# Optimization experiments

Measured on AMD Instinct MI355X. Metric: run time of the kernel, lower is better.

The kernel has to match this reference:

```python
import jax, jax.numpy as jnp
import numpy as np

N = 50000          # nodes
F = 128            # feature dim (indim = outdim)
AVG_DEG = 12       # random edges per node (plus one self-loop)
AVG_D_LOG = 2.6    # avg_d['log'] used by PNA scalers
EPS = 1e-5         # PNA std epsilon / BatchNorm eps


def setup_inputs() -> dict:
    key = jax.random.key(0)
    k1, k2, k3, k4 = jax.random.split(key, 4)
    h = jax.random.normal(k1, (N, F), dtype=jnp.float32)
    E_rand = N * AVG_DEG
    src_r = jax.random.randint(k2, (E_rand,), 0, N)
    dst_r = jax.random.randint(k3, (E_rand,), 0, N)
    loop = jnp.arange(N)
    src = jnp.concatenate([src_r, loop]).astype(jnp.int64) if jax.config.jax_enable_x64 else jnp.concatenate([src_r, loop]).astype(jnp.int32)
    dst = jnp.concatenate([dst_r, loop]).astype(src.dtype)
    concat_dim = F * (1 + 4 * 3)  # indim * (1 + n_aggr * n_scalers)
    W = jax.random.normal(k4, (concat_dim, F), dtype=jnp.float32) * (1.0 / np.sqrt(concat_dim))
    b = jnp.zeros((F,), dtype=jnp.float32)
    gamma = jnp.ones((F,), dtype=jnp.float32)
    beta = jnp.zeros((F,), dtype=jnp.float32)
    return {"h": h, "src": src, "dst": dst, "W": W, "b": b, "gamma": gamma, "beta": beta}


def _pna_forward(h, W, b, gamma, beta, src, dst):
    n = h.shape[0]
    m = h[src]                                            # [E, F] gathered mailbox
    deg = jax.ops.segment_sum(jnp.ones(src.shape[0], h.dtype), dst, num_segments=n)
    deg = jnp.maximum(deg, 1.0)[:, None]                  # every node has a self-loop
    s = jax.ops.segment_sum(m, dst, num_segments=n)
    mean = s / deg
    mx = jax.ops.segment_max(m, dst, num_segments=n)
    mn = jax.ops.segment_min(m, dst, num_segments=n)
    mean_sq = jax.ops.segment_sum(m * m, dst, num_segments=n) / deg
    std = jnp.sqrt(jax.nn.relu(mean_sq - mean * mean) + EPS)
    agg = jnp.concatenate([mean, mx, mn, std], axis=1)    # [N, 4F]
    logd = jnp.log(deg + 1.0)                             # [N, 1]
    scaled = jnp.concatenate([agg,
                              agg * (logd / AVG_D_LOG),
                              agg * (AVG_D_LOG / logd)], axis=1)  # [N, 12F]
    hc = jnp.concatenate([h, scaled], axis=1)             # [N, 13F]
    out = hc @ W + b                                      # posttrans (single linear)
    out = jax.nn.relu(out)                                # activation (dropout p=0)
    mu = out.mean(axis=0)                                 # BatchNorm1d, training stats
    var = out.var(axis=0)                                 # biased variance (torch)
    out = gamma * (out - mu) * jax.lax.rsqrt(var + EPS) + beta
    return out


def reference(h, src, dst, W, b, gamma, beta):
    return _pna_forward(h, W, b, gamma, beta, src, dst)
```

## Files before the change

kernel.cpp:

```cpp
#include <hip/hip_runtime.h>
#include <math.h>

#define FDIM 128
#define AVG_D_LOGF 2.6f
#define BN_EPS 1e-5f
#define NK 10

using f32x2 = __attribute__((ext_vector_type(2))) float;
using f32x4 = __attribute__((ext_vector_type(4))) float;
using s16x8 = __attribute__((ext_vector_type(8))) short;
using u16x8 = __attribute__((ext_vector_type(8))) unsigned short;

__device__ __forceinline__ unsigned short f2bf(float x) {
  unsigned int u = __float_as_uint(x);
  u += 0x7FFFu + ((u >> 16) & 1u);
  return (unsigned short)(u >> 16);
}
__device__ __forceinline__ float bf2f(unsigned short u) {
  return __uint_as_float(((unsigned int)u) << 16);
}
__device__ __forceinline__ f32x2 bfpair(unsigned int u) {
  union { uint2 u2; f32x2 f; } c;
  c.u2 = make_uint2(u << 16, u & 0xFFFF0000u);
  return c.f;
}

__device__ __forceinline__ void gload16(const void* g, void* l) {
  __builtin_amdgcn_global_load_lds(
      (const __attribute__((address_space(1))) void*)g,
      (__attribute__((address_space(3))) void*)l, 16, 0, 0);
}

__global__ void prep_kernel(const float* __restrict__ h, unsigned short* __restrict__ hb,
                            const float* __restrict__ W, unsigned short* __restrict__ wBT,
                            const int* __restrict__ dst, int* __restrict__ deg,
                            int w0, int w1, int w2, int K) {
  int i = blockIdx.x * 256 + threadIdx.x;
  if (i < w0) {
    const f32x4* sp = (const f32x4*)h + (size_t)i * 2;
    f32x4 v0 = sp[0], v1 = sp[1];
    u16x8 o;
    o[0] = f2bf(v0[0]); o[1] = f2bf(v0[1]); o[2] = f2bf(v0[2]); o[3] = f2bf(v0[3]);
    o[4] = f2bf(v1[0]); o[5] = f2bf(v1[1]); o[6] = f2bf(v1[2]); o[7] = f2bf(v1[3]);
    *((u16x8*)hb + i) = o;
  } else if (i < w0 + w1) {
    int idx = i - w0;
    int k = idx >> 7, j = idx & 127;
    wBT[(size_t)j * K + k] = f2bf(W[idx]);
  } else if (i < w0 + w1 + w2) {
    atomicAdd(&deg[dst[i - w0 - w1]], 1);
  }
}

__global__ void scan1(const int* __restrict__ deg, int* __restrict__ offs,
                      int* __restrict__ bsums, int n) {
  __shared__ int tmp[256];
  int t = threadIdx.x, i = blockIdx.x * 256 + t;
  int v = (i < n) ? deg[i] : 0;
  tmp[t] = v; __syncthreads();
  for (int d = 1; d < 256; d <<= 1) {
    int x = (t >= d) ? tmp[t - d] : 0;
    __syncthreads();
    tmp[t] += x;
    __syncthreads();
  }
  if (i < n) offs[i] = tmp[t] - v;
  if (t == 255) bsums[blockIdx.x] = tmp[255];
}

__global__ void csr_fill(const int* __restrict__ src, const int* __restrict__ dst,
                         const int* __restrict__ offs, const int* __restrict__ bsums,
                         int* __restrict__ cursor, int* __restrict__ csr, int E, int nb) {
  __shared__ int tmp[256];
  __shared__ int ex[256];
  const int t = threadIdx.x;
  {
    int v = (t < nb) ? bsums[t] : 0;
    tmp[t] = v; __syncthreads();
    for (int d = 1; d < 256; d <<= 1) {
      int x = (t >= d) ? tmp[t - d] : 0;
      __syncthreads();
      tmp[t] += x;
      __syncthreads();
    }
    ex[t] = tmp[t] - v;
    __syncthreads();
  }
  int i = blockIdx.x * 256 + t;
  if (i < E) {
    int d = dst[i];
    int pos = offs[d] + ex[d >> 8] + atomicAdd(&cursor[d], 1);
    csr[pos] = src[i];
  }
}

__global__ __launch_bounds__(256) void agg_kernel(
    const unsigned short* __restrict__ hb, const int* __restrict__ csr,
    const int* __restrict__ offs, const int* __restrict__ bsums,
    unsigned short* __restrict__ aggb, float2* __restrict__ s12a,
    int n, int E, int nb) {
  __shared__ int tmp[256];
  __shared__ int ex[256];
  {
    int t = threadIdx.x;
    int v = (t < nb) ? bsums[t] : 0;
    tmp[t] = v; __syncthreads();
    for (int d = 1; d < 256; d <<= 1) {
      int x = (t >= d) ? tmp[t - d] : 0;
      __syncthreads();
      tmp[t] += x;
      __syncthreads();
    }
    ex[t] = tmp[t] - v;
    __syncthreads();
  }
  const int gw = (blockIdx.x * 256 + threadIdx.x) >> 6;
  const int lane = threadIdx.x & 63;
  if (gw >= n) return;
  const int beg = offs[gw] + ex[gw >> 8];
  const int end = (gw + 1 < n) ? offs[gw + 1] + ex[(gw + 1) >> 8] : E;
  const int sub = lane >> 5;
  const int fl  = lane & 31;
  const uint2* hp2 = (const uint2*)hb;

  f32x2 s[2] = {{0.f, 0.f}, {0.f, 0.f}};
  f32x2 q[2] = {{0.f, 0.f}, {0.f, 0.f}};
  f32x2 mx[2] = {{-INFINITY, -INFINITY}, {-INFINITY, -INFINITY}};
  f32x2 mn[2] = {{INFINITY, INFINITY}, {INFINITY, INFINITY}};

  auto acc1 = [&](uint2 A) {
    f32x2 a0 = bfpair(A.x), a1 = bfpair(A.y);
    s[0] += a0; s[1] += a1;
    q[0] += a0 * a0; q[1] += a1 * a1;
    mx[0] = __builtin_elementwise_max(mx[0], a0);
    mx[1] = __builtin_elementwise_max(mx[1], a1);
    mn[0] = __builtin_elementwise_min(mn[0], a0);
    mn[1] = __builtin_elementwise_min(mn[1], a1);
  };

  const int cnt = end - beg;
  const int pairs = cnt >> 1;
  int p = 0;
  for (; p + 4 <= pairs; p += 4) {
    int base = beg + 2 * p + sub;
    int i0 = csr[base], i1 = csr[base + 2], i2 = csr[base + 4], i3 = csr[base + 6];
    uint2 A = hp2[(size_t)i0 * 32 + fl];
    uint2 B = hp2[(size_t)i1 * 32 + fl];
    uint2 C = hp2[(size_t)i2 * 32 + fl];
    uint2 D = hp2[(size_t)i3 * 32 + fl];
    acc1(A); acc1(B); acc1(C); acc1(D);
  }
  for (; p < pairs; ++p) {
    int i0 = csr[beg + 2 * p + sub];
    acc1(hp2[(size_t)i0 * 32 + fl]);
  }
  if ((cnt & 1) && sub == 0) {
    int i0 = csr[end - 1];
    acc1(hp2[(size_t)i0 * 32 + fl]);
  }

  #pragma unroll
  for (int k = 0; k < 2; ++k) {
    s[k][0] += __shfl_xor(s[k][0], 32);  s[k][1] += __shfl_xor(s[k][1], 32);
    q[k][0] += __shfl_xor(q[k][0], 32);  q[k][1] += __shfl_xor(q[k][1], 32);
    mx[k][0] = fmaxf(mx[k][0], __shfl_xor(mx[k][0], 32));
    mx[k][1] = fmaxf(mx[k][1], __shfl_xor(mx[k][1], 32));
    mn[k][0] = fminf(mn[k][0], __shfl_xor(mn[k][0], 32));
    mn[k][1] = fminf(mn[k][1], __shfl_xor(mn[k][1], 32));
  }

  float degf = (float)cnt;
  if (degf < 1.f) degf = 1.f;
  const float inv = 1.f / degf;
  if (sub == 0) {
    f32x2 me0 = s[0] * inv, me1 = s[1] * inv;
    float st0 = sqrtf(fmaxf(q[0][0] * inv - me0[0] * me0[0], 0.f) + BN_EPS);
    float st1 = sqrtf(fmaxf(q[0][1] * inv - me0[1] * me0[1], 0.f) + BN_EPS);
    float st2 = sqrtf(fmaxf(q[1][0] * inv - me1[0] * me1[0], 0.f) + BN_EPS);
    float st3 = sqrtf(fmaxf(q[1][1] * inv - me1[1] * me1[1], 0.f) + BN_EPS);
    unsigned int b = (unsigned int)gw * 512u + (unsigned int)fl * 4u;
    uint2 wme = make_uint2((unsigned int)f2bf(me0[0]) | ((unsigned int)f2bf(me0[1]) << 16),
                           (unsigned int)f2bf(me1[0]) | ((unsigned int)f2bf(me1[1]) << 16));
    uint2 wmx = make_uint2((unsigned int)f2bf(mx[0][0]) | ((unsigned int)f2bf(mx[0][1]) << 16),
                           (unsigned int)f2bf(mx[1][0]) | ((unsigned int)f2bf(mx[1][1]) << 16));
    uint2 wmn = make_uint2((unsigned int)f2bf(mn[0][0]) | ((unsigned int)f2bf(mn[0][1]) << 16),
                           (unsigned int)f2bf(mn[1][0]) | ((unsigned int)f2bf(mn[1][1]) << 16));
    uint2 wst = make_uint2((unsigned int)f2bf(st0) | ((unsigned int)f2bf(st1) << 16),
                           (unsigned int)f2bf(st2) | ((unsigned int)f2bf(st3) << 16));
    *(uint2*)&aggb[b      ] = wme;
    *(uint2*)&aggb[b + 128] = wmx;
    *(uint2*)&aggb[b + 256] = wmn;
    *(uint2*)&aggb[b + 384] = wst;
  }
  if (lane == 0) {
    float logd = logf(degf + 1.f);
    s12a[gw] = make_float2(logd / AVG_D_LOGF, AVG_D_LOGF / logd);
  }
}

__global__ __launch_bounds__(256, 3) void gemm_kernel(
    const unsigned short* __restrict__ hb, const unsigned short* __restrict__ wBT,
    const unsigned short* __restrict__ aggb, const float2* __restrict__ s12a,
    const float* __restrict__ bias, float* __restrict__ out,
    float* __restrict__ bnsum, float* __restrict__ bnsq, int n, int K) {
  __shared__ s16x8 As[1024];
  __shared__ s16x8 Bs[3][512];
  const int t = threadIdx.x;
  const int lane = t & 63;
  const int w = t >> 6;
  const int wr = w >> 1, wc = w & 1;
  const int hi = lane >> 4, lr = lane & 15, rx7 = lr & 7;

  const int nwg = gridDim.x;
  const int q = nwg >> 3, r = nwg & 7;
  const int xcd = blockIdx.x & 7, jj = blockIdx.x >> 3;
  const int bx = (xcd < r ? xcd * (q + 1) : r * (q + 1) + (xcd - r) * q) + jj;

  const int m0 = (bx >> 1) * 128;
  const int n0 = (bx & 1) * 64;

  f32x4 acc[3][4][2] = {};

  auto stage = [&](int ss) {
    const bool ph1 = (ss < 2);
    #pragma unroll
    for (int i = 0; i < 4; ++i) {
      int unit = w * 256 + i * 64 + lane;
      int row = unit >> 3, x = unit & 7;
      int node = m0 + row; if (node >= n) node = n - 1;
      int xo = (x ^ (row & 7)) << 3;
      const unsigned short* src = ph1
          ? hb   + (size_t)node * FDIM + ss * 64 + xo
          : aggb + (size_t)node * 512 + (ss - 2) * 64 + xo;
      gload16(src, &As[w * 256 + i * 64]);
    }
    const int nsec = ph1 ? 1 : 3;
    for (int s = 0; s < nsec; ++s) {
      int koff = ph1 ? ss * 64 : (FDIM + s * 512 + (ss - 2) * 64);
      #pragma unroll
      for (int i = 0; i < 2; ++i) {
        int unit = w * 128 + i * 64 + lane;
        int row = unit >> 3, x = unit & 7;
        const unsigned short* src =
            wBT + (size_t)(n0 + row) * K + koff + ((x ^ (row & 7)) << 3);
        gload16(src, &Bs[s][w * 128 + i * 64]);
      }
    }
  };

  for (int step = 0; step < NK; ++step) {
    stage(step);
    __syncthreads();
    #pragma unroll
    for (int ks = 0; ks < 2; ++ks) {
      s16x8 a[4];
      #pragma unroll
      for (int m = 0; m < 4; ++m) {
        int row = wr * 64 + m * 16 + lr;
        a[m] = As[row * 8 + ((ks * 4 + hi) ^ rx7)];
      }
      #pragma unroll
      for (int s = 0; s < 3; ++s) {
        if (step < 2 && s > 0) continue;
        int rb = wc * 32 + lr;
        s16x8 b0 = Bs[s][rb * 8 + ((ks * 4 + hi) ^ rx7)];
        s16x8 b1 = Bs[s][(rb + 16) * 8 + ((ks * 4 + hi) ^ rx7)];
        #pragma unroll
        for (int m = 0; m < 4; ++m) {
          acc[s][m][0] = __builtin_amdgcn_mfma_f32_16x16x32_bf16(a[m], b0, acc[s][m][0], 0, 0, 0);
          acc[s][m][1] = __builtin_amdgcn_mfma_f32_16x16x32_bf16(a[m], b1, acc[s][m][1], 0, 0, 0);
        }
      }
    }
    __syncthreads();
  }

  float* red = (float*)&As[0];
  if (t < 128) red[t] = 0.f;
  __syncthreads();

  const float bv0 = bias[n0 + wc * 32 + lr];
  const float bv1 = bias[n0 + wc * 32 + 16 + lr];
  float cs[2] = {0.f, 0.f}, cq[2] = {0.f, 0.f};
  #pragma unroll
  for (int m = 0; m < 4; ++m) {
    #pragma unroll
    for (int i = 0; i < 4; ++i) {
      int grow = m0 + wr * 64 + m * 16 + hi * 4 + i;
      if (grow >= n) continue;
      float2 sv = s12a[grow];
      #pragma unroll
      for (int nn = 0; nn < 2; ++nn) {
        float v = acc[0][m][nn][i] + sv.x * acc[1][m][nn][i] + sv.y * acc[2][m][nn][i]
                + (nn ? bv1 : bv0);
        v = fmaxf(v, 0.f);
        out[(size_t)grow * FDIM + n0 + wc * 32 + nn * 16 + lr] = v;
        cs[nn] += v; cq[nn] += v * v;
      }
    }
  }
  #pragma unroll
  for (int nn = 0; nn < 2; ++nn) {
    int lc = wc * 32 + nn * 16 + lr;
    atomicAdd(&red[lc], cs[nn]);
    atomicAdd(&red[64 + lc], cq[nn]);
  }
  __syncthreads();
  if (t < 64)       atomicAdd(&bnsum[n0 + t], red[t]);
  else if (t < 128) atomicAdd(&bnsq[n0 + t - 64], red[t]);
}

__global__ void bn_norm(float* __restrict__ out, const float* __restrict__ bnsum,
                        const float* __restrict__ bnsq, const float* __restrict__ gamma,
                        const float* __restrict__ beta, int n) {
  __shared__ float scs[128], shs[128];
  const int t = threadIdx.x;
  if (t < 128) {
    const float invN = 1.f / (float)n;
    const float mu = bnsum[t] * invN;
    const float var = bnsq[t] * invN - mu * mu;
    const float rs = rsqrtf(var + BN_EPS);
    const float s = gamma[t] * rs;
    scs[t] = s; shs[t] = beta[t] - mu * s;
  }
  __syncthreads();
  const int total = n * 32;
  int idx = blockIdx.x * 256 + t;
  const int c4 = (idx & 31) * 4;
  const float s0 = scs[c4], s1 = scs[c4 + 1], s2 = scs[c4 + 2], s3 = scs[c4 + 3];
  const float h0 = shs[c4], h1 = shs[c4 + 1], h2 = shs[c4 + 2], h3 = shs[c4 + 3];
  for (; idx < total; idx += gridDim.x * 256) {
    f32x4 v = ((f32x4*)out)[idx];
    v[0] = v[0] * s0 + h0;
    v[1] = v[1] * s1 + h1;
    v[2] = v[2] * s2 + h2;
    v[3] = v[3] * s3 + h3;
    ((f32x4*)out)[idx] = v;
  }
}

extern "C" void kernel_launch(void* const* d_in, const int* in_sizes, int n_in,
                              void* d_out, int out_size, void* d_ws, size_t ws_size,
                              hipStream_t stream) {
  const float* h     = (const float*)d_in[0];
  const int*   src   = (const int*)d_in[1];
  const int*   dst   = (const int*)d_in[2];
  const float* W     = (const float*)d_in[3];
  const float* bias  = (const float*)d_in[4];
  const float* gamma = (const float*)d_in[5];
  const float* beta  = (const float*)d_in[6];
  float* out = (float*)d_out;

  const int n = in_sizes[0] / FDIM;
  const int E = in_sizes[1];
  const int K = in_sizes[3] / FDIM;

  char* base = (char*)d_ws;
  size_t off = 0;
  auto alloc = [&](size_t bytes) -> void* {
    void* p = base + off;
    off += (bytes + 255) & ~(size_t)255;
    return p;
  };
  int*   deg    = (int*)  alloc(4ull * n);
  int*   cursor = (int*)  alloc(4ull * n);
  float* bnsum  = (float*)alloc(512);
  float* bnsq   = (float*)alloc(512);
  const size_t zlen = off;
  int*    offs  = (int*)  alloc(4ull * (n + 1));
  int*    bsums = (int*)  alloc(4ull * 256);
  int*    csr   = (int*)  alloc(4ull * E);
  float2* s12a  = (float2*)alloc(8ull * n);
  unsigned short* aggb = (unsigned short*)alloc(2ull * (size_t)n * 512);
  unsigned short* wBT  = (unsigned short*)alloc(2ull * (size_t)K * FDIM);
  unsigned short* hb   = (unsigned short*)alloc(2ull * (size_t)n * FDIM);
  (void)ws_size; (void)n_in; (void)out_size;

  const int eb = (E + 255) / 256;
  const int nb = (n + 255) / 256;
  const int w0 = n * FDIM / 8;
  const int w1 = K * FDIM;
  const int w2 = E;

  hipMemsetAsync(d_ws, 0, zlen, stream);
  prep_kernel<<<(w0 + w1 + w2 + 255) / 256, 256, 0, stream>>>(h, hb, W, wBT, dst, deg,
                                                              w0, w1, w2, K);
  scan1<<<nb, 256, 0, stream>>>(deg, offs, bsums, n);
  csr_fill<<<eb, 256, 0, stream>>>(src, dst, offs, bsums, cursor, csr, E, nb);
  agg_kernel<<<(n + 3) / 4, 256, 0, stream>>>(hb, csr, offs, bsums, aggb, s12a, n, E, nb);
  const int gblocks = ((n + 127) / 128) * 2;
  gemm_kernel<<<gblocks, 256, 0, stream>>>(hb, wBT, aggb, s12a, bias,
                                           out, bnsum, bnsq, n, K);
  bn_norm<<<2048, 256, 0, stream>>>(out, bnsum, bnsq, gamma, beta, n);
}
```

Baseline: 181.4 us.

## Double-buffer GEMM LDS stages and prescale CSR indices for cheaper gathers

The GEMM kernel now double-buffers its A/B shared-memory tiles, issuing the next stage's global-to-LDS loads before computing the current one, with manual vmcnt waits and raw barriers in place of __syncthreads. Occupancy hint drops from 3 to 2 blocks per CU because LDS use doubles. Separately, the CSR stores source indices pre-shifted to byte offsets, so the aggregation gather avoids index multiplication, and the accumulators use inline packed add/fma asm. Risks: hand-counted vmcnt values must match the number of issued loads per stage, and the shifted indices could overflow for very large node counts.

```diff
diff --git a/kernel.cpp b/kernel.cpp
--- a/kernel.cpp
+++ b/kernel.cpp
@@ -90,7 +90,7 @@
   if (i < E) {
     int d = dst[i];
     int pos = offs[d] + ex[d >> 8] + atomicAdd(&cursor[d], 1);
-    csr[pos] = src[i];
+    csr[pos] = src[i] << 8;
   }
 }
 
@@ -121,21 +121,26 @@
   const int end = (gw + 1 < n) ? offs[gw + 1] + ex[(gw + 1) >> 8] : E;
   const int sub = lane >> 5;
   const int fl  = lane & 31;
-  const uint2* hp2 = (const uint2*)hb;
-
-  f32x2 s[2] = {{0.f, 0.f}, {0.f, 0.f}};
-  f32x2 q[2] = {{0.f, 0.f}, {0.f, 0.f}};
-  f32x2 mx[2] = {{-INFINITY, -INFINITY}, {-INFINITY, -INFINITY}};
-  f32x2 mn[2] = {{INFINITY, INFINITY}, {INFINITY, INFINITY}};
+  const char* hbase = (const char*)hb + fl * 8;
+
+  f32x2 s0v = {0.f, 0.f}, s1v = {0.f, 0.f};
+  f32x2 q0v = {0.f, 0.f}, q1v = {0.f, 0.f};
+  f32x2 mx0 = {-INFINITY, -INFINITY}, mx1 = {-INFINITY, -INFINITY};
+  f32x2 mn0 = {INFINITY, INFINITY},  mn1 = {INFINITY, INFINITY};
 
   auto acc1 = [&](uint2 A) {
     f32x2 a0 = bfpair(A.x), a1 = bfpair(A.y);
-    s[0] += a0; s[1] += a1;
-    q[0] += a0 * a0; q[1] += a1 * a1;
-    mx[0] = __builtin_elementwise_max(mx[0], a0);
-    mx[1] = __builtin_elementwise_max(mx[1], a1);
-    mn[0] = __builtin_elementwise_min(mn[0], a0);
-    mn[1] = __builtin_elementwise_min(mn[1], a1);
+    asm("v_pk_add_f32 %0, %0, %1" : "+v"(s0v) : "v"(a0));
+    asm("v_pk_add_f32 %0, %0, %1" : "+v"(s1v) : "v"(a1));
+    asm("v_pk_fma_f32 %0, %1, %1, %0" : "+v"(q0v) : "v"(a0));
+    asm("v_pk_fma_f32 %0, %1, %1, %0" : "+v"(q1v) : "v"(a1));
+    mx0[0] = fmaxf(mx0[0], a0[0]); mx0[1] = fmaxf(mx0[1], a0[1]);
+    mx1[0] = fmaxf(mx1[0], a1[0]); mx1[1] = fmaxf(mx1[1], a1[1]);
+    mn0[0] = fminf(mn0[0], a0[0]); mn0[1] = fminf(mn0[1], a0[1]);
+    mn1[0] = fminf(mn1[0], a1[0]); mn1[1] = fminf(mn1[1], a1[1]);
+  };
+  auto gat = [&](int byteoff) -> uint2 {
+    return *(const uint2*)(hbase + byteoff);
   };
 
   const int cnt = end - beg;
@@ -144,47 +149,41 @@
   for (; p + 4 <= pairs; p += 4) {
     int base = beg + 2 * p + sub;
     int i0 = csr[base], i1 = csr[base + 2], i2 = csr[base + 4], i3 = csr[base + 6];
-    uint2 A = hp2[(size_t)i0 * 32 + fl];
-    uint2 B = hp2[(size_t)i1 * 32 + fl];
-    uint2 C = hp2[(size_t)i2 * 32 + fl];
-    uint2 D = hp2[(size_t)i3 * 32 + fl];
+    uint2 A = gat(i0), B = gat(i1), C = gat(i2), D = gat(i3);
     acc1(A); acc1(B); acc1(C); acc1(D);
   }
   for (; p < pairs; ++p) {
-    int i0 = csr[beg + 2 * p + sub];
-    acc1(hp2[(size_t)i0 * 32 + fl]);
+    acc1(gat(csr[beg + 2 * p + sub]));
   }
   if ((cnt & 1) && sub == 0) {
-    int i0 = csr[end - 1];
-    acc1(hp2[(size_t)i0 * 32 + fl]);
-  }
-
-  #pragma unroll
-  for (int k = 0; k < 2; ++k) {
-    s[k][0] += __shfl_xor(s[k][0], 32);  s[k][1] += __shfl_xor(s[k][1], 32);
-    q[k][0] += __shfl_xor(q[k][0], 32);  q[k][1] += __shfl_xor(q[k][1], 32);
-    mx[k][0] = fmaxf(mx[k][0], __shfl_xor(mx[k][0], 32));
-    mx[k][1] = fmaxf(mx[k][1], __shfl_xor(mx[k][1], 32));
-    mn[k][0] = fminf(mn[k][0], __shfl_xor(mn[k][0], 32));
-    mn[k][1] = fminf(mn[k][1], __shfl_xor(mn[k][1], 32));
-  }
+    acc1(gat(csr[end - 1]));
+  }
+
+  s0v[0] += __shfl_xor(s0v[0], 32); s0v[1] += __shfl_xor(s0v[1], 32);
+  s1v[0] += __shfl_xor(s1v[0], 32); s1v[1] += __shfl_xor(s1v[1], 32);
+  q0v[0] += __shfl_xor(q0v[0], 32); q0v[1] += __shfl_xor(q0v[1], 32);
+  q1v[0] += __shfl_xor(q1v[0], 32); q1v[1] += __shfl_xor(q1v[1], 32);
+  mx0[0] = fmaxf(mx0[0], __shfl_xor(mx0[0], 32)); mx0[1] = fmaxf(mx0[1], __shfl_xor(mx0[1], 32));
+  mx1[0] = fmaxf(mx1[0], __shfl_xor(mx1[0], 32)); mx1[1] = fmaxf(mx1[1], __shfl_xor(mx1[1], 32));
+  mn0[0] = fminf(mn0[0], __shfl_xor(mn0[0], 32)); mn0[1] = fminf(mn0[1], __shfl_xor(mn0[1], 32));
+  mn1[0] = fminf(mn1[0], __shfl_xor(mn1[0], 32)); mn1[1] = fminf(mn1[1], __shfl_xor(mn1[1], 32));
 
   float degf = (float)cnt;
   if (degf < 1.f) degf = 1.f;
   const float inv = 1.f / degf;
   if (sub == 0) {
-    f32x2 me0 = s[0] * inv, me1 = s[1] * inv;
-    float st0 = sqrtf(fmaxf(q[0][0] * inv - me0[0] * me0[0], 0.f) + BN_EPS);
-    float st1 = sqrtf(fmaxf(q[0][1] * inv - me0[1] * me0[1], 0.f) + BN_EPS);
-    float st2 = sqrtf(fmaxf(q[1][0] * inv - me1[0] * me1[0], 0.f) + BN_EPS);
-    float st3 = sqrtf(fmaxf(q[1][1] * inv - me1[1] * me1[1], 0.f) + BN_EPS);
+    float me0 = s0v[0] * inv, me1 = s0v[1] * inv, me2 = s1v[0] * inv, me3 = s1v[1] * inv;
+    float st0 = sqrtf(fmaxf(q0v[0] * inv - me0 * me0, 0.f) + BN_EPS);
+    float st1 = sqrtf(fmaxf(q0v[1] * inv - me1 * me1, 0.f) + BN_EPS);
+    float st2 = sqrtf(fmaxf(q1v[0] * inv - me2 * me2, 0.f) + BN_EPS);
+    float st3 = sqrtf(fmaxf(q1v[1] * inv - me3 * me3, 0.f) + BN_EPS);
     unsigned int b = (unsigned int)gw * 512u + (unsigned int)fl * 4u;
-    uint2 wme = make_uint2((unsigned int)f2bf(me0[0]) | ((unsigned int)f2bf(me0[1]) << 16),
-                           (unsigned int)f2bf(me1[0]) | ((unsigned int)f2bf(me1[1]) << 16));
-    uint2 wmx = make_uint2((unsigned int)f2bf(mx[0][0]) | ((unsigned int)f2bf(mx[0][1]) << 16),
-                           (unsigned int)f2bf(mx[1][0]) | ((unsigned int)f2bf(mx[1][1]) << 16));
-    uint2 wmn = make_uint2((unsigned int)f2bf(mn[0][0]) | ((unsigned int)f2bf(mn[0][1]) << 16),
-                           (unsigned int)f2bf(mn[1][0]) | ((unsigned int)f2bf(mn[1][1]) << 16));
+    uint2 wme = make_uint2((unsigned int)f2bf(me0) | ((unsigned int)f2bf(me1) << 16),
+                           (unsigned int)f2bf(me2) | ((unsigned int)f2bf(me3) << 16));
+    uint2 wmx = make_uint2((unsigned int)f2bf(mx0[0]) | ((unsigned int)f2bf(mx0[1]) << 16),
+                           (unsigned int)f2bf(mx1[0]) | ((unsigned int)f2bf(mx1[1]) << 16));
+    uint2 wmn = make_uint2((unsigned int)f2bf(mn0[0]) | ((unsigned int)f2bf(mn0[1]) << 16),
+                           (unsigned int)f2bf(mn1[0]) | ((unsigned int)f2bf(mn1[1]) << 16));
     uint2 wst = make_uint2((unsigned int)f2bf(st0) | ((unsigned int)f2bf(st1) << 16),
                            (unsigned int)f2bf(st2) | ((unsigned int)f2bf(st3) << 16));
     *(uint2*)&aggb[b      ] = wme;
@@ -198,13 +197,13 @@
   }
 }
 
-__global__ __launch_bounds__(256, 3) void gemm_kernel(
+__global__ __launch_bounds__(256, 2) void gemm_kernel(
     const unsigned short* __restrict__ hb, const unsigned short* __restrict__ wBT,
     const unsigned short* __restrict__ aggb, const float2* __restrict__ s12a,
     const float* __restrict__ bias, float* __restrict__ out,
     float* __restrict__ bnsum, float* __restrict__ bnsq, int n, int K) {
-  __shared__ s16x8 As[1024];
-  __shared__ s16x8 Bs[3][512];
+  __shared__ s16x8 AsB[2][1024];
+  __shared__ s16x8 BsB[2][3][512];
   const int t = threadIdx.x;
   const int lane = t & 63;
   const int w = t >> 6;
@@ -221,7 +220,7 @@
 
   f32x4 acc[3][4][2] = {};
 
-  auto stage = [&](int ss) {
+  auto stage = [&](int ss, int buf) {
     const bool ph1 = (ss < 2);
     #pragma unroll
     for (int i = 0; i < 4; ++i) {
@@ -232,7 +231,7 @@
       const unsigned short* src = ph1
           ? hb   + (size_t)node * FDIM + ss * 64 + xo
           : aggb + (size_t)node * 512 + (ss - 2) * 64 + xo;
-      gload16(src, &As[w * 256 + i * 64]);
+      gload16(src, &AsB[buf][w * 256 + i * 64]);
     }
     const int nsec = ph1 ? 1 : 3;
     for (int s = 0; s < nsec; ++s) {
@@ -243,28 +242,36 @@
         int row = unit >> 3, x = unit & 7;
         const unsigned short* src =
             wBT + (size_t)(n0 + row) * K + koff + ((x ^ (row & 7)) << 3);
-        gload16(src, &Bs[s][w * 128 + i * 64]);
+        gload16(src, &BsB[buf][s][w * 128 + i * 64]);
       }
     }
   };
 
+  stage(0, 0);
+  int cur = 0;
   for (int step = 0; step < NK; ++step) {
-    stage(step);
-    __syncthreads();
+    if (step + 1 < NK) {
+      stage(step + 1, cur ^ 1);
+      if (step + 1 < 2) asm volatile("s_waitcnt vmcnt(6)" ::: "memory");
+      else              asm volatile("s_waitcnt vmcnt(10)" ::: "memory");
+    } else {
+      asm volatile("s_waitcnt vmcnt(0)" ::: "memory");
+    }
+    asm volatile("s_barrier" ::: "memory");
     #pragma unroll
     for (int ks = 0; ks < 2; ++ks) {
       s16x8 a[4];
       #pragma unroll
       for (int m = 0; m < 4; ++m) {
         int row = wr * 64 + m * 16 + lr;
-        a[m] = As[row * 8 + ((ks * 4 + hi) ^ rx7)];
+        a[m] = AsB[cur][row * 8 + ((ks * 4 + hi) ^ rx7)];
       }
       #pragma unroll
       for (int s = 0; s < 3; ++s) {
         if (step < 2 && s > 0) continue;
         int rb = wc * 32 + lr;
-        s16x8 b0 = Bs[s][rb * 8 + ((ks * 4 + hi) ^ rx7)];
-        s16x8 b1 = Bs[s][(rb + 16) * 8 + ((ks * 4 + hi) ^ rx7)];
+        s16x8 b0 = BsB[cur][s][rb * 8 + ((ks * 4 + hi) ^ rx7)];
+        s16x8 b1 = BsB[cur][s][(rb + 16) * 8 + ((ks * 4 + hi) ^ rx7)];
         #pragma unroll
         for (int m = 0; m < 4; ++m) {
           acc[s][m][0] = __builtin_amdgcn_mfma_f32_16x16x32_bf16(a[m], b0, acc[s][m][0], 0, 0, 0);
@@ -272,10 +279,11 @@
         }
       }
     }
-    __syncthreads();
-  }
-
-  float* red = (float*)&As[0];
+    asm volatile("s_barrier" ::: "memory");
+    cur ^= 1;
+  }
+
+  float* red = (float*)&AsB[0][0];
   if (t < 128) red[t] = 0.f;
   __syncthreads();
 
```

New measurement: 175.1 us. 1.04x faster.
